# Performance work log

Hardware: AMD Instinct MI355X
Metric: run time of the kernel (lower is better)

Reference implementation:

```python
import jax, jax.numpy as jnp
import numpy as np

N = 100000   # nodes
E = 1600000  # edges per graph (avg degree 16)
H = 32       # hidden_dim
L = 5        # num_layers
NEG_SLOPE = 0.2
PRELU_W = 0.1


def setup_inputs() -> dict:
    key = jax.random.key(0)
    ks = jax.random.split(key, 32)
    nrm = lambda k, s: jax.random.normal(k, s, dtype=jnp.float32) * 0.1
    inp = {
        "x": jax.random.normal(ks[0], (N, 1), dtype=jnp.float32),
        "source_edge_index": jax.random.randint(ks[1], (2, E), 0, N, dtype=jnp.int64) if jax.config.jax_enable_x64 else jax.random.randint(ks[1], (2, E), 0, N, dtype=jnp.int32),
        "sink_edge_index": jax.random.randint(ks[2], (2, E), 0, N, dtype=jnp.int32),
        "W_in_src": nrm(ks[3], (1, H)), "b_in_src": nrm(ks[4], (H,)),
        "a1_in_src": nrm(ks[5], (H,)), "a2_in_src": nrm(ks[6], (H,)),
        "W_in_snk": nrm(ks[7], (1, H)), "b_in_snk": nrm(ks[8], (H,)),
        "a1_in_snk": nrm(ks[9], (H,)), "a2_in_snk": nrm(ks[10], (H,)),
        "W_src": nrm(ks[11], (L - 1, H, H)), "b_src": nrm(ks[12], (L - 1, H)),
        "a1_src": nrm(ks[13], (L - 1, H)), "a2_src": nrm(ks[14], (L - 1, H)),
        "W_snk": nrm(ks[15], (L - 1, H, H)), "b_snk": nrm(ks[16], (L - 1, H)),
        "a1_snk": nrm(ks[17], (L - 1, H)), "a2_snk": nrm(ks[18], (L - 1, H)),
        "W_o_src": nrm(ks[19], (2 * H, 2)), "b_o_src": nrm(ks[20], (2,)),
        "W_o_snk": nrm(ks[21], (2 * H, 2)), "b_o_snk": nrm(ks[22], (2,)),
        "W_d1": nrm(ks[23], (2 * H, 2)), "b_d1": nrm(ks[24], (2,)),
    }
    return inp


def _prelu(v):
    return jnp.where(v >= 0, v, PRELU_W * v)


def _gat(xf, ei, W, b, a1, a2):
    # single-head GATConv, concat=False: linear -> edge attention softmax over dst -> scatter-add
    h = xf @ W                                   # [N,H]
    s, d = ei[0], ei[1]
    e = jax.nn.leaky_relu((h @ a1)[s] + (h @ a2)[d], NEG_SLOPE)   # [E]
    m = jax.ops.segment_max(e, d, num_segments=N)
    m = jnp.where(jnp.isfinite(m), m, 0.0)
    p = jnp.exp(e - m[d])
    denom = jax.ops.segment_sum(p, d, num_segments=N)
    alpha = p / (denom[d] + 1e-16)
    out = jax.ops.segment_sum(alpha[:, None] * h[s], d, num_segments=N)
    return out + b


def _edge_neighbor(emb, ei, filt):
    # message: x_j * filt[src]; aggr='add'; update: aggr + emb/2
    s, d = ei[0], ei[1]
    agg = jax.ops.segment_sum(emb[s] * filt[s], d, num_segments=N)
    return agg + emb / 2


def reference(x, source_edge_index, sink_edge_index,
              W_in_src, b_in_src, a1_in_src, a2_in_src,
              W_in_snk, b_in_snk, a1_in_snk, a2_in_snk,
              W_src, b_src, a1_src, a2_src,
              W_snk, b_snk, a1_snk, a2_snk,
              W_o_src, b_o_src, W_o_snk, b_o_snk, W_d1, b_d1):
    # eval mode: dropout is identity
    se = _prelu(_gat(x, source_edge_index, W_in_src, b_in_src, a1_in_src, a2_in_src))
    sk = _prelu(_gat(x, sink_edge_index, W_in_snk, b_in_snk, a1_in_snk, a2_in_snk))
    for i in range(L - 1):
        c = se + sk   # combine='add'
        se = _prelu(_gat(c, source_edge_index, W_src[i], b_src[i], a1_src[i], a2_src[i]))
        sk = _prelu(_gat(c, sink_edge_index, W_snk[i], b_snk[i], a1_snk[i], a2_snk[i]))
    comb = jnp.concatenate([se, sk], axis=-1)     # [N, 2H] to match Linear(2H, 2)
    s0 = jax.nn.relu(comb @ W_o_src + b_o_src)
    k0 = jax.nn.relu(comb @ W_o_snk + b_o_snk)
    final_dim0 = (s0 + k0) / 2                    # [N, 2]
    e1s = jax.nn.relu(_edge_neighbor(comb, source_edge_index, x))
    e1k = jax.nn.relu(_edge_neighbor(comb, sink_edge_index, x))
    final_dim1 = jax.nn.relu((e1s + e1k) @ W_d1 + b_d1)   # [N, 2]
    return jnp.concatenate([final_dim0, final_dim1], axis=1)  # [N, 4]
```

## Files before the change

kernel.cpp:

```cpp
#include <hip/hip_runtime.h>

#define NEG_SLOPE 0.2f
#define PRELU_W 0.1f

__device__ __forceinline__ float d_lrelu(float v){ return fmaxf(v, NEG_SLOPE * v); }
__device__ __forceinline__ float d_prelu(float v){ return fmaxf(v, PRELU_W * v); }

__device__ __forceinline__ unsigned short f2bf(float f){
  unsigned int u = __builtin_bit_cast(unsigned int, f);
  unsigned int r = (u + 0x7fffu + ((u >> 16) & 1u)) >> 16;
  return (unsigned short)r;
}
__device__ __forceinline__ float bflo(unsigned int u){ return __builtin_bit_cast(float, u << 16); }
__device__ __forceinline__ float bfhi(unsigned int u){ return __builtin_bit_cast(float, u & 0xffff0000u); }


__global__ void k_zero(int* __restrict__ p, int n){
  int i = blockIdx.x * 256 + threadIdx.x;
  if (i < n) p[i] = 0;
}

__global__ void k_count_rank(const int* __restrict__ eiS, const int* __restrict__ eiK,
                             int* __restrict__ degS, int* __restrict__ degK,
                             int* __restrict__ rankS, int* __restrict__ rankK, int E){
  int e0 = blockIdx.x * 512 + threadIdx.x;
  int e1 = e0 + 256;
  bool v0 = e0 < E, v1 = e1 < E;
  int dS0 = 0, dK0 = 0, dS1 = 0, dK1 = 0;
  if (v0){ dS0 = eiS[E + e0]; dK0 = eiK[E + e0]; }
  if (v1){ dS1 = eiS[E + e1]; dK1 = eiK[E + e1]; }
  if (v0){
    rankS[e0] = atomicAdd(&degS[dS0], 1);
    rankK[e0] = atomicAdd(&degK[dK0], 1);
  }
  if (v1){
    rankS[e1] = atomicAdd(&degS[dS1], 1);
    rankK[e1] = atomicAdd(&degK[dK1], 1);
  }
}

__global__ void k_scan1(const int* __restrict__ degS, const int* __restrict__ degK,
                        int* __restrict__ bsumS, int* __restrict__ bsumK, int n){
  const int* deg = blockIdx.y ? degK : degS;
  int* bsum = blockIdx.y ? bsumK : bsumS;
  int b = blockIdx.x, t = threadIdx.x;
  int base = b * 1024 + t * 4;
  int s = 0;
  #pragma unroll
  for (int k2 = 0; k2 < 4; ++k2){ int i = base + k2; if (i < n) s += deg[i]; }
  #pragma unroll
  for (int d = 32; d >= 1; d >>= 1) s += __shfl_xor(s, d, 64);
  __shared__ int ws[4];
  int lane = t & 63, wid = t >> 6;
  if (lane == 0) ws[wid] = s;
  __syncthreads();
  if (t == 0) bsum[b] = ws[0] + ws[1] + ws[2] + ws[3];
}

__global__ void k_scan2(int* __restrict__ bsumS, int* __restrict__ bsumK, int nb,
                        int* __restrict__ rsS, int* __restrict__ rsK, int n){
  int* bsum = blockIdx.x ? bsumK : bsumS;
  int* rs = blockIdx.x ? rsK : rsS;
  int t = threadIdx.x;
  int v = (t < nb) ? bsum[t] : 0;
  int x = v;
  int lane = t & 63, wid = t >> 6;
  #pragma unroll
  for (int d = 1; d < 64; d <<= 1){ int y = __shfl_up(x, d, 64); if (lane >= d) x += y; }
  __shared__ int wq[2];
  if (lane == 63) wq[wid] = x;
  __syncthreads();
  if (wid == 1) x += wq[0];
  if (t < nb) bsum[t] = x - v;
  if (t == nb - 1) rs[n] = x;
}

__global__ void k_scan3(const int* __restrict__ degS, const int* __restrict__ degK,
                        const int* __restrict__ bsumS, const int* __restrict__ bsumK,
                        int* __restrict__ rsS, int* __restrict__ rsK, int n){
  const int* deg = blockIdx.y ? degK : degS;
  const int* bsum = blockIdx.y ? bsumK : bsumS;
  int* rs = blockIdx.y ? rsK : rsS;
  int b = blockIdx.x, t = threadIdx.x;
  int base = b * 1024 + t * 4;
  int v[4];
  #pragma unroll
  for (int k2 = 0; k2 < 4; ++k2){ int i = base + k2; v[k2] = (i < n) ? deg[i] : 0; }
  int tsum = v[0] + v[1] + v[2] + v[3];
  int x = tsum;
  int lane = t & 63, wid = t >> 6;
  #pragma unroll
  for (int d = 1; d < 64; d <<= 1){ int y = __shfl_up(x, d, 64); if (lane >= d) x += y; }
  __shared__ int ws[4];
  if (lane == 63) ws[wid] = x;
  __syncthreads();
  int woff = 0;
  for (int w = 0; w < wid; ++w) woff += ws[w];
  int run = bsum[b] + woff + (x - tsum);
  #pragma unroll
  for (int k2 = 0; k2 < 4; ++k2){ int i = base + k2; if (i < n) rs[i] = run; run += v[k2]; }
}

__global__ void k_place(const int* __restrict__ eiS, const int* __restrict__ eiK,
                        const int* __restrict__ rsS, const int* __restrict__ rsK,
                        const int* __restrict__ rankS, const int* __restrict__ rankK,
                        int* __restrict__ colS, int* __restrict__ colK, int E){
  int e0 = blockIdx.x * 512 + threadIdx.x;
  int e1 = e0 + 256;
  bool v0 = e0 < E, v1 = e1 < E;
  if (v0){
    int sS = eiS[e0], dS = eiS[E + e0];
    int sK = eiK[e0], dK = eiK[E + e0];
    int rS = rankS[e0], rK = rankK[e0];
    colS[rsS[dS] + rS] = sS;
    colK[rsK[dK] + rK] = sK;
  }
  if (v1){
    int sS = eiS[e1], dS = eiS[E + e1];
    int sK = eiK[e1], dK = eiK[E + e1];
    int rS = rankS[e1], rK = rankK[e1];
    colS[rsS[dS] + rS] = sS;
    colK[rsK[dK] + rK] = sK;
  }
}

__global__ void k_gat_l1(const int* __restrict__ rsA, const int* __restrict__ colA,
                         const int* __restrict__ rsB, const int* __restrict__ colB,
                         const float* __restrict__ x,
                         const float* __restrict__ WA, const float* __restrict__ bA,
                         const float* __restrict__ a1A, const float* __restrict__ a2A,
                         const float* __restrict__ WB, const float* __restrict__ bB,
                         const float* __restrict__ a1B, const float* __restrict__ a2B,
                         float* __restrict__ outA, float* __restrict__ outB, int n){
  bool g = (blockIdx.y != 0);
  const int* rs  = g ? rsB  : rsA;
  const int* col = g ? colB : colA;
  const float* W = g ? WB : WA;  const float* bias = g ? bB : bA;
  const float* a1 = g ? a1B : a1A; const float* a2 = g ? a2B : a2A;
  float* outp = g ? outB : outA;

  __shared__ float sp[2];
  int t = threadIdx.x;
  if (t < 32){
    float wk = W[t];
    float q1 = wk * a1[t], q2 = wk * a2[t];
    #pragma unroll
    for (int d = 16; d >= 1; d >>= 1){ q1 += __shfl_xor(q1, d, 32); q2 += __shfl_xor(q2, d, 32); }
    if (t == 0){ sp[0] = q1; sp[1] = q2; }
  }
  __syncthreads();
  float p1 = sp[0], p2 = sp[1];

  int gid = blockIdx.x * 256 + t;
  int node = gid >> 3, l8 = gid & 7;
  if (node >= n) return;
  float a2d = x[node] * p2;
  int beg = rs[node], end = rs[node + 1];
  float denom = 0.f, accx = 0.f;
  #pragma unroll 2
  for (int idx = beg + l8; idx < end; idx += 8){
    float xs = x[col[idx]];
    float w = __expf(d_lrelu(xs * p1 + a2d));
    denom += w;
    accx += w * xs;
  }
  #pragma unroll
  for (int d = 4; d >= 1; d >>= 1){
    denom += __shfl_xor(denom, d, 8);
    accx  += __shfl_xor(accx,  d, 8);
  }
  float r = accx / (denom + 1e-16f);
  float4 Wv = *(const float4*)(W + l8 * 4);
  float4 Bv = *(const float4*)(bias + l8 * 4);
  float4 o;
  o.x = d_prelu(r * Wv.x + Bv.x);
  o.y = d_prelu(r * Wv.y + Bv.y);
  o.z = d_prelu(r * Wv.z + Bv.z);
  o.w = d_prelu(r * Wv.w + Bv.w);
  *(float4*)(outp + (size_t)node * 32 + l8 * 4) = o;
}

__global__ void k_linear(const float* __restrict__ se, const float* __restrict__ sk,
                         const float* __restrict__ WS, const float* __restrict__ WK,
                         const float* __restrict__ a1S, const float* __restrict__ a2S,
                         const float* __restrict__ a1K, const float* __restrict__ a2K,
                         unsigned short* __restrict__ hS, unsigned short* __restrict__ hK,
                         float* __restrict__ oa1S, float* __restrict__ oa2S,
                         float* __restrict__ oa1K, float* __restrict__ oa2K, int n){
  __shared__ float sWS[1024], sWK[1024], sa[128];
  int t = threadIdx.x;
  for (int i = t; i < 1024; i += 256){ sWS[i] = WS[i]; sWK[i] = WK[i]; }
  if (t < 32){ sa[t] = a1S[t]; sa[32 + t] = a2S[t]; sa[64 + t] = a1K[t]; sa[96 + t] = a2K[t]; }
  __syncthreads();
  int gid = blockIdx.x * 256 + t;
  int node = gid >> 5, k = gid & 31;
  if (node >= n) return;
  float c = se[node * 32 + k] + sk[node * 32 + k];
  float hs = 0.f, hk = 0.f;
  #pragma unroll
  for (int m = 0; m < 32; ++m){
    float cm = __shfl(c, m, 32);
    hs += cm * sWS[m * 32 + k];
    hk += cm * sWK[m * 32 + k];
  }
  hS[node * 32 + k] = f2bf(hs);
  hK[node * 32 + k] = f2bf(hk);
  float r1 = hs * sa[k], r2 = hs * sa[32 + k], r3 = hk * sa[64 + k], r4 = hk * sa[96 + k];
  #pragma unroll
  for (int d = 16; d >= 1; d >>= 1){
    r1 += __shfl_xor(r1, d, 32); r2 += __shfl_xor(r2, d, 32);
    r3 += __shfl_xor(r3, d, 32); r4 += __shfl_xor(r4, d, 32);
  }
  if (k == 0){ oa1S[node] = r1; oa2S[node] = r2; oa1K[node] = r3; oa2K[node] = r4; }
}

__global__ void k_gat_agg(const int* __restrict__ rsA, const int* __restrict__ colA,
                          const unsigned short* __restrict__ hA,
                          const float* __restrict__ a1A, const float* __restrict__ a2A,
                          const float* __restrict__ bA, float* __restrict__ outA,
                          const int* __restrict__ rsB, const int* __restrict__ colB,
                          const unsigned short* __restrict__ hB,
                          const float* __restrict__ a1B, const float* __restrict__ a2B,
                          const float* __restrict__ bB, float* __restrict__ outB, int n){
  bool g2 = (blockIdx.y != 0);
  const int* rs  = g2 ? rsB  : rsA;
  const int* col = g2 ? colB : colA;
  const unsigned short* h = g2 ? hB : hA;
  const float* a1 = g2 ? a1B : a1A;
  const float* a2 = g2 ? a2B : a2A;
  const float* bias = g2 ? bB : bA;
  float* outp = g2 ? outB : outA;

  int t = threadIdx.x;
  int lane = t & 63;
  int half = lane >> 5, l32 = lane & 31;
  int node = blockIdx.x * 8 + (t >> 6) * 2 + half;
  if (node >= n) return;
  int g = l32 >> 2;
  int k = (l32 & 3) * 8;
  float a2d = a2[node];
  int beg = rs[node], end = rs[node + 1];
  float acc[8] = {0.f,0.f,0.f,0.f,0.f,0.f,0.f,0.f};
  float dpart = 0.f;
  #pragma unroll 2
  for (int idx = beg + g; idx < end; idx += 8){
    int s = col[idx];
    float w = __expf(d_lrelu(a1[s] + a2d));
    uint4 hv = *(const uint4*)(h + (((size_t)s) << 5) + k);
    dpart += w;
    acc[0] += w * bflo(hv.x); acc[1] += w * bfhi(hv.x);
    acc[2] += w * bflo(hv.y); acc[3] += w * bfhi(hv.y);
    acc[4] += w * bflo(hv.z); acc[5] += w * bfhi(hv.z);
    acc[6] += w * bflo(hv.w); acc[7] += w * bfhi(hv.w);
  }
  #pragma unroll
  for (int m = 4; m <= 16; m <<= 1){
    #pragma unroll
    for (int i = 0; i < 8; ++i) acc[i] += __shfl_xor(acc[i], m, 32);
    dpart += __shfl_xor(dpart, m, 32);
  }
  if (g == 0){
    float inv = 1.f / (dpart + 1e-16f);
    float4 b0 = *(const float4*)(bias + k);
    float4 b1 = *(const float4*)(bias + k + 4);
    float4 o0, o1;
    o0.x = d_prelu(acc[0] * inv + b0.x);
    o0.y = d_prelu(acc[1] * inv + b0.y);
    o0.z = d_prelu(acc[2] * inv + b0.z);
    o0.w = d_prelu(acc[3] * inv + b0.w);
    o1.x = d_prelu(acc[4] * inv + b1.x);
    o1.y = d_prelu(acc[5] * inv + b1.y);
    o1.z = d_prelu(acc[6] * inv + b1.z);
    o1.w = d_prelu(acc[7] * inv + b1.w);
    *(float4*)(outp + (size_t)node * 32 + k) = o0;
    *(float4*)(outp + (size_t)node * 32 + k + 4) = o1;
  }
}

__global__ void k_head0(const float* __restrict__ se, const float* __restrict__ sk,
                        const float* __restrict__ Wos, const float* __restrict__ bos,
                        const float* __restrict__ Wok, const float* __restrict__ bok,
                        unsigned short* __restrict__ comb, float* __restrict__ outp, int n){
  int gid = blockIdx.x * 256 + threadIdx.x;
  int node = gid >> 6, k = gid & 63;
  if (node >= n) return;
  float cv = (k < 32) ? se[node * 32 + k] : sk[node * 32 + (k - 32)];
  comb[(size_t)node * 64 + k] = f2bf(cv);
  float s0 = cv * Wos[k * 2], s1 = cv * Wos[k * 2 + 1];
  float q0 = cv * Wok[k * 2], q1 = cv * Wok[k * 2 + 1];
  #pragma unroll
  for (int d = 32; d >= 1; d >>= 1){
    s0 += __shfl_xor(s0, d, 64); s1 += __shfl_xor(s1, d, 64);
    q0 += __shfl_xor(q0, d, 64); q1 += __shfl_xor(q1, d, 64);
  }
  if (k == 0){
    float f0 = (fmaxf(s0 + bos[0], 0.f) + fmaxf(q0 + bok[0], 0.f)) * 0.5f;
    float f1 = (fmaxf(s1 + bos[1], 0.f) + fmaxf(q1 + bok[1], 0.f)) * 0.5f;
    outp[node * 4 + 0] = f0;
    outp[node * 4 + 1] = f1;
  }
}

__global__ void k_head1(const int* __restrict__ rsS, const int* __restrict__ colS,
                        const int* __restrict__ rsK, const int* __restrict__ colK,
                        const unsigned short* __restrict__ comb, const float* __restrict__ x,
                        const float* __restrict__ Wd1, const float* __restrict__ bd1,
                        float* __restrict__ outp, int n){
  int lane = threadIdx.x & 63;
  int node = blockIdx.x * 4 + (threadIdx.x >> 6);
  if (node >= n) return;
  int g8 = lane >> 3, k8 = (lane & 7) * 8;
  float aS[8] = {0.f,0.f,0.f,0.f,0.f,0.f,0.f,0.f};
  float aK[8] = {0.f,0.f,0.f,0.f,0.f,0.f,0.f,0.f};
  {
    int beg = rsS[node], end = rsS[node + 1];
    #pragma unroll 2
    for (int idx = beg + g8; idx < end; idx += 8){
      int s = colS[idx];
      float xs = x[s];
      uint4 cv = *(const uint4*)(comb + (((size_t)s) << 6) + k8);
      aS[0] += xs * bflo(cv.x); aS[1] += xs * bfhi(cv.x);
      aS[2] += xs * bflo(cv.y); aS[3] += xs * bfhi(cv.y);
      aS[4] += xs * bflo(cv.z); aS[5] += xs * bfhi(cv.z);
      aS[6] += xs * bflo(cv.w); aS[7] += xs * bfhi(cv.w);
    }
  }
  {
    int beg = rsK[node], end = rsK[node + 1];
    #pragma unroll 2
    for (int idx = beg + g8; idx < end; idx += 8){
      int s = colK[idx];
      float xs = x[s];
      uint4 cv = *(const uint4*)(comb + (((size_t)s) << 6) + k8);
      aK[0] += xs * bflo(cv.x); aK[1] += xs * bfhi(cv.x);
      aK[2] += xs * bflo(cv.y); aK[3] += xs * bfhi(cv.y);
      aK[4] += xs * bflo(cv.z); aK[5] += xs * bfhi(cv.z);
      aK[6] += xs * bflo(cv.w); aK[7] += xs * bfhi(cv.w);
    }
  }
  #pragma unroll
  for (int m = 8; m <= 32; m <<= 1){
    #pragma unroll
    for (int i = 0; i < 8; ++i){
      aS[i] += __shfl_xor(aS[i], m, 64);
      aK[i] += __shfl_xor(aK[i], m, 64);
    }
  }
  uint4 cs = *(const uint4*)(comb + (((size_t)node) << 6) + k8);
  float c[8] = { bflo(cs.x), bfhi(cs.x), bflo(cs.y), bfhi(cs.y),
                 bflo(cs.z), bfhi(cs.z), bflo(cs.w), bfhi(cs.w) };
  float r0 = 0.f, r1 = 0.f;
  #pragma unroll
  for (int i = 0; i < 8; ++i){
    float cd = c[i] * 0.5f;
    float tv = fmaxf(aS[i] + cd, 0.f) + fmaxf(aK[i] + cd, 0.f);
    float2 w = *(const float2*)(Wd1 + (k8 + i) * 2);
    r0 += tv * w.x;
    r1 += tv * w.y;
  }
  #pragma unroll
  for (int m = 1; m <= 4; m <<= 1){
    r0 += __shfl_xor(r0, m, 64);
    r1 += __shfl_xor(r1, m, 64);
  }
  if (lane == 0){
    outp[(size_t)node * 4 + 2] = fmaxf(r0 + bd1[0], 0.f);
    outp[(size_t)node * 4 + 3] = fmaxf(r1 + bd1[1], 0.f);
  }
}


extern "C" void kernel_launch(void* const* d_in, const int* in_sizes, int n_in,
                              void* d_out, int out_size, void* d_ws, size_t ws_size,
                              hipStream_t stream) {
  const float* x      = (const float*)d_in[0];
  const int*   eiS    = (const int*)d_in[1];
  const int*   eiK    = (const int*)d_in[2];
  const float* W_in_src = (const float*)d_in[3];
  const float* b_in_src = (const float*)d_in[4];
  const float* a1_in_src= (const float*)d_in[5];
  const float* a2_in_src= (const float*)d_in[6];
  const float* W_in_snk = (const float*)d_in[7];
  const float* b_in_snk = (const float*)d_in[8];
  const float* a1_in_snk= (const float*)d_in[9];
  const float* a2_in_snk= (const float*)d_in[10];
  const float* W_src  = (const float*)d_in[11];
  const float* b_src  = (const float*)d_in[12];
  const float* a1_src = (const float*)d_in[13];
  const float* a2_src = (const float*)d_in[14];
  const float* W_snk  = (const float*)d_in[15];
  const float* b_snk  = (const float*)d_in[16];
  const float* a1_snk = (const float*)d_in[17];
  const float* a2_snk = (const float*)d_in[18];
  const float* W_o_src= (const float*)d_in[19];
  const float* b_o_src= (const float*)d_in[20];
  const float* W_o_snk= (const float*)d_in[21];
  const float* b_o_snk= (const float*)d_in[22];
  const float* W_d1   = (const float*)d_in[23];
  const float* b_d1   = (const float*)d_in[24];
  float* outp = (float*)d_out;

  const int N = in_sizes[0];
  const int E = in_sizes[1] / 2;
  const int L = 5;

  float* f = (float*)d_ws;
  float* seA = f;  f += (size_t)N * 32;
  float* skA = f;  f += (size_t)N * 32;
  float* a1Sv = f; f += N;
  float* a2Sv = f; f += N;
  float* a1Kv = f; f += N;
  float* a2Kv = f; f += N;
  int* ip = (int*)f;
  int* rsS    = ip; ip += N + 4;
  int* rsK    = ip; ip += N + 4;
  int* colS   = ip; ip += E;
  int* colK   = ip; ip += E;
  int* degS   = ip; ip += N;
  int* degK   = ip; ip += N;
  int* bsumS  = ip; ip += 256;
  int* bsumK  = ip; ip += 256;
  unsigned short* us = (unsigned short*)ip;
  unsigned short* hS   = us; us += (size_t)N * 32;
  unsigned short* hK   = us; us += (size_t)N * 32;
  unsigned short* comb = us; us += (size_t)N * 64;
  int* rankS = (int*)hS;
  int* rankK = (int*)hK;

  const int TB = 256;
  int gE2   = (E + 511) / 512;
  int gN32  = (N * 32 + TB - 1) / TB;
  int gN64  = (N * 64 + TB - 1) / TB;
  int gN8   = (N * 8 + TB - 1) / TB;
  int gNode4 = (N + 3) / 4;
  int gNode8 = (N + 7) / 8;
  int nb    = (N + 1023) / 1024;

  hipLaunchKernelGGL(k_zero,  dim3((2 * N + TB - 1) / TB), dim3(TB), 0, stream, degS, 2 * N);
  hipLaunchKernelGGL(k_count_rank, dim3(gE2), dim3(TB), 0, stream,
                     eiS, eiK, degS, degK, rankS, rankK, E);
  hipLaunchKernelGGL(k_scan1, dim3(nb, 2), dim3(TB), 0, stream, degS, degK, bsumS, bsumK, N);
  hipLaunchKernelGGL(k_scan2, dim3(2), dim3(128), 0, stream, bsumS, bsumK, nb, rsS, rsK, N);
  hipLaunchKernelGGL(k_scan3, dim3(nb, 2), dim3(TB), 0, stream,
                     degS, degK, bsumS, bsumK, rsS, rsK, N);
  hipLaunchKernelGGL(k_place, dim3(gE2), dim3(TB), 0, stream,
                     eiS, eiK, rsS, rsK, rankS, rankK, colS, colK, E);

  hipLaunchKernelGGL(k_gat_l1, dim3(gN8, 2), dim3(TB), 0, stream,
                     rsS, colS, rsK, colK, x,
                     W_in_src, b_in_src, a1_in_src, a2_in_src,
                     W_in_snk, b_in_snk, a1_in_snk, a2_in_snk,
                     seA, skA, N);

  for (int i = 0; i < L - 1; ++i){
    hipLaunchKernelGGL(k_linear, dim3(gN32), dim3(TB), 0, stream,
                       seA, skA, W_src + (size_t)i * 1024, W_snk + (size_t)i * 1024,
                       a1_src + i * 32, a2_src + i * 32, a1_snk + i * 32, a2_snk + i * 32,
                       hS, hK, a1Sv, a2Sv, a1Kv, a2Kv, N);
    hipLaunchKernelGGL(k_gat_agg, dim3(gNode8, 2), dim3(TB), 0, stream,
                       rsS, colS, hS, a1Sv, a2Sv, b_src + i * 32, seA,
                       rsK, colK, hK, a1Kv, a2Kv, b_snk + i * 32, skA, N);
  }

  hipLaunchKernelGGL(k_head0, dim3(gN64), dim3(TB), 0, stream,
                     seA, skA, W_o_src, b_o_src, W_o_snk, b_o_snk, comb, outp, N);
  hipLaunchKernelGGL(k_head1, dim3(gNode4), dim3(TB), 0, stream,
                     rsS, colS, rsK, colK, comb, x, W_d1, b_d1, outp, N);
}
```

Before: 851.8 us.

## Partition CSR build atomics by destination range per XCD and drop rank arrays

Reworks the CSR construction. Each block now handles one of eight destination-node ranges, so the atomics for a given range come from a predictable subset of blocks, which the block-index mapping presumably ties to one XCD for cache locality. The rank arrays are gone: the placement kernel uses atomic cursors that the scan initialises to the row starts. Each block now reads edges eight times over, and the order of neighbours within a row becomes nondeterministic.

```diff
diff --git a/kernel.cpp b/kernel.cpp
--- a/kernel.cpp
+++ b/kernel.cpp
@@ -20,22 +20,23 @@
   if (i < n) p[i] = 0;
 }
 
-__global__ void k_count_rank(const int* __restrict__ eiS, const int* __restrict__ eiK,
-                             int* __restrict__ degS, int* __restrict__ degK,
-                             int* __restrict__ rankS, int* __restrict__ rankK, int E){
-  int e0 = blockIdx.x * 512 + threadIdx.x;
-  int e1 = e0 + 256;
-  bool v0 = e0 < E, v1 = e1 < E;
-  int dS0 = 0, dK0 = 0, dS1 = 0, dK1 = 0;
-  if (v0){ dS0 = eiS[E + e0]; dK0 = eiK[E + e0]; }
-  if (v1){ dS1 = eiS[E + e1]; dK1 = eiK[E + e1]; }
-  if (v0){
-    rankS[e0] = atomicAdd(&degS[dS0], 1);
-    rankK[e0] = atomicAdd(&degK[dK0], 1);
-  }
-  if (v1){
-    rankS[e1] = atomicAdd(&degS[dS1], 1);
-    rankK[e1] = atomicAdd(&degK[dK1], 1);
+__global__ void k_count_x(const int* __restrict__ eiS, const int* __restrict__ eiK,
+                          int* __restrict__ degS, int* __restrict__ degK,
+                          int E, int rngN, int n){
+  int r = blockIdx.x & 7;
+  int c = blockIdx.x >> 3;
+  int lo = r * rngN;
+  int hi = min(lo + rngN, n);
+  int base = c * 2048 + threadIdx.x;
+  #pragma unroll
+  for (int i = 0; i < 8; ++i){
+    int e = base + i * 256;
+    if (e < E){
+      int dS = eiS[E + e];
+      if (dS >= lo && dS < hi) atomicAdd(&degS[dS], 1);
+      int dK = eiK[E + e];
+      if (dK >= lo && dK < hi) atomicAdd(&degK[dK], 1);
+    }
   }
 }
 
@@ -75,10 +76,10 @@
   if (t == nb - 1) rs[n] = x;
 }
 
-__global__ void k_scan3(const int* __restrict__ degS, const int* __restrict__ degK,
+__global__ void k_scan3(int* __restrict__ degS, int* __restrict__ degK,
                         const int* __restrict__ bsumS, const int* __restrict__ bsumK,
                         int* __restrict__ rsS, int* __restrict__ rsK, int n){
-  const int* deg = blockIdx.y ? degK : degS;
+  int* deg = blockIdx.y ? degK : degS;
   const int* bsum = blockIdx.y ? bsumK : bsumS;
   int* rs = blockIdx.y ? rsK : rsS;
   int b = blockIdx.x, t = threadIdx.x;
@@ -98,29 +99,37 @@
   for (int w = 0; w < wid; ++w) woff += ws[w];
   int run = bsum[b] + woff + (x - tsum);
   #pragma unroll
-  for (int k2 = 0; k2 < 4; ++k2){ int i = base + k2; if (i < n) rs[i] = run; run += v[k2]; }
-}
-
-__global__ void k_place(const int* __restrict__ eiS, const int* __restrict__ eiK,
-                        const int* __restrict__ rsS, const int* __restrict__ rsK,
-                        const int* __restrict__ rankS, const int* __restrict__ rankK,
-                        int* __restrict__ colS, int* __restrict__ colK, int E){
-  int e0 = blockIdx.x * 512 + threadIdx.x;
-  int e1 = e0 + 256;
-  bool v0 = e0 < E, v1 = e1 < E;
-  if (v0){
-    int sS = eiS[e0], dS = eiS[E + e0];
-    int sK = eiK[e0], dK = eiK[E + e0];
-    int rS = rankS[e0], rK = rankK[e0];
-    colS[rsS[dS] + rS] = sS;
-    colK[rsK[dK] + rK] = sK;
-  }
-  if (v1){
-    int sS = eiS[e1], dS = eiS[E + e1];
-    int sK = eiK[e1], dK = eiK[E + e1];
-    int rS = rankS[e1], rK = rankK[e1];
-    colS[rsS[dS] + rS] = sS;
-    colK[rsK[dK] + rK] = sK;
+  for (int k2 = 0; k2 < 4; ++k2){
+    int i = base + k2;
+    if (i < n){ rs[i] = run; deg[i] = run; }
+    run += v[k2];
+  }
+}
+
+__global__ void k_place_x(const int* __restrict__ eiS, const int* __restrict__ eiK,
+                          int* __restrict__ curS, int* __restrict__ curK,
+                          int* __restrict__ colS, int* __restrict__ colK,
+                          int E, int rngN, int n){
+  int r = blockIdx.x & 7;
+  int c = blockIdx.x >> 3;
+  int lo = r * rngN;
+  int hi = min(lo + rngN, n);
+  int base = c * 2048 + threadIdx.x;
+  #pragma unroll
+  for (int i = 0; i < 8; ++i){
+    int e = base + i * 256;
+    if (e < E){
+      int dS = eiS[E + e];
+      if (dS >= lo && dS < hi){
+        int p = atomicAdd(&curS[dS], 1);
+        colS[p] = eiS[e];
+      }
+      int dK = eiK[E + e];
+      if (dK >= lo && dK < hi){
+        int p = atomicAdd(&curK[dK], 1);
+        colK[p] = eiK[e];
+      }
+    }
   }
 }
 
@@ -424,11 +433,10 @@
   unsigned short* hS   = us; us += (size_t)N * 32;
   unsigned short* hK   = us; us += (size_t)N * 32;
   unsigned short* comb = us; us += (size_t)N * 64;
-  int* rankS = (int*)hS;
-  int* rankK = (int*)hK;
 
   const int TB = 256;
-  int gE2   = (E + 511) / 512;
+  int rngN  = (N + 7) / 8;
+  int gCX   = ((E + 2047) / 2048) * 8;
   int gN32  = (N * 32 + TB - 1) / TB;
   int gN64  = (N * 64 + TB - 1) / TB;
   int gN8   = (N * 8 + TB - 1) / TB;
@@ -437,14 +445,14 @@
   int nb    = (N + 1023) / 1024;
 
   hipLaunchKernelGGL(k_zero,  dim3((2 * N + TB - 1) / TB), dim3(TB), 0, stream, degS, 2 * N);
-  hipLaunchKernelGGL(k_count_rank, dim3(gE2), dim3(TB), 0, stream,
-                     eiS, eiK, degS, degK, rankS, rankK, E);
+  hipLaunchKernelGGL(k_count_x, dim3(gCX), dim3(TB), 0, stream,
+                     eiS, eiK, degS, degK, E, rngN, N);
   hipLaunchKernelGGL(k_scan1, dim3(nb, 2), dim3(TB), 0, stream, degS, degK, bsumS, bsumK, N);
   hipLaunchKernelGGL(k_scan2, dim3(2), dim3(128), 0, stream, bsumS, bsumK, nb, rsS, rsK, N);
   hipLaunchKernelGGL(k_scan3, dim3(nb, 2), dim3(TB), 0, stream,
                      degS, degK, bsumS, bsumK, rsS, rsK, N);
-  hipLaunchKernelGGL(k_place, dim3(gE2), dim3(TB), 0, stream,
-                     eiS, eiK, rsS, rsK, rankS, rankK, colS, colK, E);
+  hipLaunchKernelGGL(k_place_x, dim3(gCX), dim3(TB), 0, stream,
+                     eiS, eiK, degS, degK, colS, colK, E, rngN, N);
 
   hipLaunchKernelGGL(k_gat_l1, dim3(gN8, 2), dim3(TB), 0, stream,
                      rsS, colS, rsK, colK, x,
```

Result: slower. 942.5 us (+10.7%).

## Partition degree-count atomics by destination range across block groups

Applied to the files above, without the earlier changes.

The in-degree counting and rank kernel now launches eight blocks per 2048-edge chunk. Each of the eight handles only destinations in one of eight node ranges, so each block's atomics land in a narrower slice of the degree array. This is meant to keep the atomic targets local to a cache or XCD and cut cross-die atomic contention. In exchange, every edge index is read eight times and most threads do nothing for a given edge.

```diff
diff --git a/kernel.cpp b/kernel.cpp
--- a/kernel.cpp
+++ b/kernel.cpp
@@ -20,22 +20,24 @@
   if (i < n) p[i] = 0;
 }
 
-__global__ void k_count_rank(const int* __restrict__ eiS, const int* __restrict__ eiK,
-                             int* __restrict__ degS, int* __restrict__ degK,
-                             int* __restrict__ rankS, int* __restrict__ rankK, int E){
-  int e0 = blockIdx.x * 512 + threadIdx.x;
-  int e1 = e0 + 256;
-  bool v0 = e0 < E, v1 = e1 < E;
-  int dS0 = 0, dK0 = 0, dS1 = 0, dK1 = 0;
-  if (v0){ dS0 = eiS[E + e0]; dK0 = eiK[E + e0]; }
-  if (v1){ dS1 = eiS[E + e1]; dK1 = eiK[E + e1]; }
-  if (v0){
-    rankS[e0] = atomicAdd(&degS[dS0], 1);
-    rankK[e0] = atomicAdd(&degK[dK0], 1);
-  }
-  if (v1){
-    rankS[e1] = atomicAdd(&degS[dS1], 1);
-    rankK[e1] = atomicAdd(&degK[dK1], 1);
+__global__ void k_count_rank_x(const int* __restrict__ eiS, const int* __restrict__ eiK,
+                               int* __restrict__ degS, int* __restrict__ degK,
+                               int* __restrict__ rankS, int* __restrict__ rankK,
+                               int E, int rngN, int n){
+  int r = blockIdx.x & 7;
+  int c = blockIdx.x >> 3;
+  int lo = r * rngN;
+  int hi = min(lo + rngN, n);
+  int base = c * 2048 + threadIdx.x;
+  #pragma unroll
+  for (int i = 0; i < 8; ++i){
+    int e = base + i * 256;
+    if (e < E){
+      int dS = eiS[E + e];
+      if (dS >= lo && dS < hi) rankS[e] = atomicAdd(&degS[dS], 1);
+      int dK = eiK[E + e];
+      if (dK >= lo && dK < hi) rankK[e] = atomicAdd(&degK[dK], 1);
+    }
   }
 }
 
@@ -428,6 +430,8 @@
   int* rankK = (int*)hK;
 
   const int TB = 256;
+  int rngN  = (N + 7) / 8;
+  int gCX   = ((E + 2047) / 2048) * 8;
   int gE2   = (E + 511) / 512;
   int gN32  = (N * 32 + TB - 1) / TB;
   int gN64  = (N * 64 + TB - 1) / TB;
@@ -437,8 +441,8 @@
   int nb    = (N + 1023) / 1024;
 
   hipLaunchKernelGGL(k_zero,  dim3((2 * N + TB - 1) / TB), dim3(TB), 0, stream, degS, 2 * N);
-  hipLaunchKernelGGL(k_count_rank, dim3(gE2), dim3(TB), 0, stream,
-                     eiS, eiK, degS, degK, rankS, rankK, E);
+  hipLaunchKernelGGL(k_count_rank_x, dim3(gCX), dim3(TB), 0, stream,
+                     eiS, eiK, degS, degK, rankS, rankK, E, rngN, N);
   hipLaunchKernelGGL(k_scan1, dim3(nb, 2), dim3(TB), 0, stream, degS, degK, bsumS, bsumK, N);
   hipLaunchKernelGGL(k_scan2, dim3(2), dim3(128), 0, stream, bsumS, bsumK, nb, rsS, rsK, N);
   hipLaunchKernelGGL(k_scan3, dim3(nb, 2), dim3(TB), 0, stream,
```

Result: no change. 857.8 us (+0.7%).

## Stage block edge indices and attention weights in LDS before gather

Applied to the files above, without the earlier changes.

The GAT aggregation and head1 neighbor kernels now load each block's contiguous CSR edge segment cooperatively. One thread per edge reads the column index and computes the attention weight (or x value) once, and stores them in shared memory. Each half-wave then reads those from LDS while gathering feature rows. Before, every one of the four lanes per edge recomputed the exp and reloaded col and a1. This removes that redundant global and transcendental work and coalesces the index reads, at the cost of extra __syncthreads and LDS traffic.

```diff
diff --git a/kernel.cpp b/kernel.cpp
--- a/kernel.cpp
+++ b/kernel.cpp
@@ -214,66 +214,103 @@
   if (k == 0){ oa1S[node] = r1; oa2S[node] = r2; oa1K[node] = r3; oa2K[node] = r4; }
 }
 
-__global__ void k_gat_agg(const int* __restrict__ rsA, const int* __restrict__ colA,
-                          const unsigned short* __restrict__ hA,
-                          const float* __restrict__ a1A, const float* __restrict__ a2A,
-                          const float* __restrict__ bA, float* __restrict__ outA,
-                          const int* __restrict__ rsB, const int* __restrict__ colB,
-                          const unsigned short* __restrict__ hB,
-                          const float* __restrict__ a1B, const float* __restrict__ a2B,
-                          const float* __restrict__ bB, float* __restrict__ outB, int n){
-  bool g2 = (blockIdx.y != 0);
-  const int* rs  = g2 ? rsB  : rsA;
-  const int* col = g2 ? colB : colA;
-  const unsigned short* h = g2 ? hB : hA;
-  const float* a1 = g2 ? a1B : a1A;
-  const float* a2 = g2 ? a2B : a2A;
-  const float* bias = g2 ? bB : bA;
-  float* outp = g2 ? outB : outA;
+__global__ void k_gat_agg2(const int* __restrict__ rsA, const int* __restrict__ colA,
+                           const unsigned short* __restrict__ hA,
+                           const float* __restrict__ a1A, const float* __restrict__ a2A,
+                           const float* __restrict__ bA, float* __restrict__ outA,
+                           const int* __restrict__ rsB, const int* __restrict__ colB,
+                           const unsigned short* __restrict__ hB,
+                           const float* __restrict__ a1B, const float* __restrict__ a2B,
+                           const float* __restrict__ bB, float* __restrict__ outB, int n){
+  bool gB = (blockIdx.y != 0);
+  const int* rs  = gB ? rsB  : rsA;
+  const int* col = gB ? colB : colA;
+  const unsigned short* h = gB ? hB : hA;
+  const float* a1 = gB ? a1B : a1A;
+  const float* a2 = gB ? a2B : a2A;
+  const float* bias = gB ? bB : bA;
+  float* outp = gB ? outB : outA;
+
+  __shared__ int rsL[9];
+  __shared__ int sC[256];
+  __shared__ float wC[256];
 
   int t = threadIdx.x;
+  int n0 = blockIdx.x * 8;
+  if (t < 9){
+    int idx = n0 + t;
+    rsL[t] = rs[idx < n ? idx : n];
+  }
+  __syncthreads();
+  int seg0 = rsL[0], segEnd = rsL[8];
+
   int lane = t & 63;
   int half = lane >> 5, l32 = lane & 31;
-  int node = blockIdx.x * 8 + (t >> 6) * 2 + half;
-  if (node >= n) return;
+  int nl = (t >> 6) * 2 + half;
+  int node = n0 + nl;
   int g = l32 >> 2;
   int k = (l32 & 3) * 8;
-  float a2d = a2[node];
-  int beg = rs[node], end = rs[node + 1];
+  int myBeg = rsL[nl], myEnd = rsL[nl + 1];
+  int deg = myEnd - myBeg;
+  float a2d = (node < n) ? a2[node] : 0.f;
+
   float acc[8] = {0.f,0.f,0.f,0.f,0.f,0.f,0.f,0.f};
   float dpart = 0.f;
-  #pragma unroll 2
-  for (int idx = beg + g; idx < end; idx += 8){
-    int s = col[idx];
-    float w = __expf(d_lrelu(a1[s] + a2d));
-    uint4 hv = *(const uint4*)(h + (((size_t)s) << 5) + k);
-    dpart += w;
-    acc[0] += w * bflo(hv.x); acc[1] += w * bfhi(hv.x);
-    acc[2] += w * bflo(hv.y); acc[3] += w * bfhi(hv.y);
-    acc[4] += w * bflo(hv.z); acc[5] += w * bfhi(hv.z);
-    acc[6] += w * bflo(hv.w); acc[7] += w * bfhi(hv.w);
-  }
+
+  for (int base = seg0; base < segEnd; base += 256){
+    int j = base + t;
+    int sv = 0; float wv = 0.f;
+    bool val = j < segEnd;
+    if (val){
+      sv = col[j];
+      int dl = 0;
+      #pragma unroll
+      for (int i = 1; i < 8; ++i) dl += (j >= rsL[i]);
+      wv = __expf(d_lrelu(a1[sv] + a2[n0 + dl]));
+    }
+    __syncthreads();
+    if (val){ sC[t] = sv; wC[t] = wv; }
+    __syncthreads();
+    int lo = (myBeg > base) ? myBeg : base;
+    int hi = (myEnd < base + 256) ? myEnd : (base + 256);
+    int o0 = lo - myBeg;
+    int r8 = o0 & 7;
+    int ord = o0 + ((g - r8) & 7);
+    #pragma unroll 2
+    for (; myBeg + ord < hi; ord += 8){
+      int li = myBeg + ord - base;
+      int s = sC[li];
+      float w = wC[li];
+      uint4 hv = *(const uint4*)(h + (((size_t)s) << 5) + k);
+      dpart += w;
+      acc[0] += w * bflo(hv.x); acc[1] += w * bfhi(hv.x);
+      acc[2] += w * bflo(hv.y); acc[3] += w * bfhi(hv.y);
+      acc[4] += w * bflo(hv.z); acc[5] += w * bfhi(hv.z);
+      acc[6] += w * bflo(hv.w); acc[7] += w * bfhi(hv.w);
+    }
+  }
+
   #pragma unroll
   for (int m = 4; m <= 16; m <<= 1){
     #pragma unroll
     for (int i = 0; i < 8; ++i) acc[i] += __shfl_xor(acc[i], m, 32);
     dpart += __shfl_xor(dpart, m, 32);
   }
-  if (g == 0){
+  if (g == 0 && node < n){
     float inv = 1.f / (dpart + 1e-16f);
     float4 b0 = *(const float4*)(bias + k);
     float4 b1 = *(const float4*)(bias + k + 4);
-    float4 o0, o1;
-    o0.x = d_prelu(acc[0] * inv + b0.x);
-    o0.y = d_prelu(acc[1] * inv + b0.y);
-    o0.z = d_prelu(acc[2] * inv + b0.z);
-    o0.w = d_prelu(acc[3] * inv + b0.w);
-    o1.x = d_prelu(acc[4] * inv + b1.x);
-    o1.y = d_prelu(acc[5] * inv + b1.y);
-    o1.z = d_prelu(acc[6] * inv + b1.z);
-    o1.w = d_prelu(acc[7] * inv + b1.w);
-    *(float4*)(outp + (size_t)node * 32 + k) = o0;
-    *(float4*)(outp + (size_t)node * 32 + k + 4) = o1;
+    float4 o0v, o1v;
+    o0v.x = d_prelu(acc[0] * inv + b0.x);
+    o0v.y = d_prelu(acc[1] * inv + b0.y);
+    o0v.z = d_prelu(acc[2] * inv + b0.z);
+    o0v.w = d_prelu(acc[3] * inv + b0.w);
+    o1v.x = d_prelu(acc[4] * inv + b1.x);
+    o1v.y = d_prelu(acc[5] * inv + b1.y);
+    o1v.z = d_prelu(acc[6] * inv + b1.z);
+    o1v.w = d_prelu(acc[7] * inv + b1.w);
+    *(float4*)(outp + (size_t)node * 32 + k) = o0v;
+    *(float4*)(outp + (size_t)node * 32 + k + 4) = o1v;
   }
 }
 
@@ -301,43 +338,64 @@
   }
 }
 
-__global__ void k_head1(const int* __restrict__ rsS, const int* __restrict__ colS,
-                        const int* __restrict__ rsK, const int* __restrict__ colK,
-                        const unsigned short* __restrict__ comb, const float* __restrict__ x,
-                        const float* __restrict__ Wd1, const float* __restrict__ bd1,
-                        float* __restrict__ outp, int n){
-  int lane = threadIdx.x & 63;
-  int node = blockIdx.x * 4 + (threadIdx.x >> 6);
-  if (node >= n) return;
+__global__ void k_head1b(const int* __restrict__ rsS, const int* __restrict__ colS,
+                         const int* __restrict__ rsK, const int* __restrict__ colK,
+                         const unsigned short* __restrict__ comb, const float* __restrict__ x,
+                         const float* __restrict__ Wd1, const float* __restrict__ bd1,
+                         float* __restrict__ outp, int n){
+  __shared__ int rsL[5];
+  __shared__ int sC[256];
+  __shared__ float xC[256];
+
+  int t = threadIdx.x;
+  int n0 = blockIdx.x * 4;
+  int lane = t & 63;
+  int nl = t >> 6;
+  int node = n0 + nl;
   int g8 = lane >> 3, k8 = (lane & 7) * 8;
+
   float aS[8] = {0.f,0.f,0.f,0.f,0.f,0.f,0.f,0.f};
   float aK[8] = {0.f,0.f,0.f,0.f,0.f,0.f,0.f,0.f};
-  {
-    int beg = rsS[node], end = rsS[node + 1];
-    #pragma unroll 2
-    for (int idx = beg + g8; idx < end; idx += 8){
-      int s = colS[idx];
-      float xs = x[s];
-      uint4 cv = *(const uint4*)(comb + (((size_t)s) << 6) + k8);
-      aS[0] += xs * bflo(cv.x); aS[1] += xs * bfhi(cv.x);
-      aS[2] += xs * bflo(cv.y); aS[3] += xs * bfhi(cv.y);
-      aS[4] += xs * bflo(cv.z); aS[5] += xs * bfhi(cv.z);
-      aS[6] += xs * bflo(cv.w); aS[7] += xs * bfhi(cv.w);
-    }
-  }
-  {
-    int beg = rsK[node], end = rsK[node + 1];
-    #pragma unroll 2
-    for (int idx = beg + g8; idx < end; idx += 8){
-      int s = colK[idx];
-      float xs = x[s];
-      uint4 cv = *(const uint4*)(comb + (((size_t)s) << 6) + k8);
-      aK[0] += xs * bflo(cv.x); aK[1] += xs * bfhi(cv.x);
-      aK[2] += xs * bflo(cv.y); aK[3] += xs * bfhi(cv.y);
-      aK[4] += xs * bflo(cv.z); aK[5] += xs * bfhi(cv.z);
-      aK[6] += xs * bflo(cv.w); aK[7] += xs * bfhi(cv.w);
-    }
-  }
+
+  for (int gr = 0; gr < 2; ++gr){
+    const int* rs  = gr ? rsK : rsS;
+    const int* col = gr ? colK : colS;
+    float* acc = gr ? aK : aS;
+    __syncthreads();
+    if (t < 5){
+      int idx = n0 + t;
+      rsL[t] = rs[idx < n ? idx : n];
+    }
+    __syncthreads();
+    int seg0 = rsL[0], segEnd = rsL[4];
+    int myBeg = rsL[nl], myEnd = rsL[nl + 1];
+    for (int base = seg0; base < segEnd; base += 256){
+      int j = base + t;
+      int sv = 0; float xv = 0.f;
+      bool val = j < segEnd;
+      if (val){ sv = col[j]; xv = x[sv]; }
+      __syncthreads();
+      if (val){ sC[t] = sv; xC[t] = xv; }
+      __syncthreads();
+      int lo = (myBeg > base) ? myBeg : base;
+      int hi = (myEnd < base + 256) ? myEnd : (base + 256);
+      int o0 = lo - myBeg;
+      int r8 = o0 & 7;
+      int ord = o0 + ((g8 - r8) & 7);
+      #pragma unroll 2
+      for (; myBeg + ord < hi; ord += 8){
+        int li = myBeg + ord - base;
+        int s = sC[li];
+        float xs = xC[li];
+        uint4 cv = *(const uint4*)(comb + (((size_t)s) << 6) + k8);
+        acc[0] += xs * bflo(cv.x); acc[1] += xs * bfhi(cv.x);
+        acc[2] += xs * bflo(cv.y); acc[3] += xs * bfhi(cv.y);
+        acc[4] += xs * bflo(cv.z); acc[5] += xs * bfhi(cv.z);
+        acc[6] += xs * bflo(cv.w); acc[7] += xs * bfhi(cv.w);
+      }
+    }
+  }
+
   #pragma unroll
   for (int m = 8; m <= 32; m <<= 1){
     #pragma unroll
@@ -346,26 +404,28 @@
       aK[i] += __shfl_xor(aK[i], m, 64);
     }
   }
-  uint4 cs = *(const uint4*)(comb + (((size_t)node) << 6) + k8);
-  float c[8] = { bflo(cs.x), bfhi(cs.x), bflo(cs.y), bfhi(cs.y),
-                 bflo(cs.z), bfhi(cs.z), bflo(cs.w), bfhi(cs.w) };
-  float r0 = 0.f, r1 = 0.f;
-  #pragma unroll
-  for (int i = 0; i < 8; ++i){
-    float cd = c[i] * 0.5f;
-    float tv = fmaxf(aS[i] + cd, 0.f) + fmaxf(aK[i] + cd, 0.f);
-    float2 w = *(const float2*)(Wd1 + (k8 + i) * 2);
-    r0 += tv * w.x;
-    r1 += tv * w.y;
-  }
-  #pragma unroll
-  for (int m = 1; m <= 4; m <<= 1){
-    r0 += __shfl_xor(r0, m, 64);
-    r1 += __shfl_xor(r1, m, 64);
-  }
-  if (lane == 0){
-    outp[(size_t)node * 4 + 2] = fmaxf(r0 + bd1[0], 0.f);
-    outp[(size_t)node * 4 + 3] = fmaxf(r1 + bd1[1], 0.f);
+  if (node < n){
+    uint4 cs = *(const uint4*)(comb + (((size_t)node) << 6) + k8);
+    float c[8] = { bflo(cs.x), bfhi(cs.x), bflo(cs.y), bfhi(cs.y),
+                   bflo(cs.z), bfhi(cs.z), bflo(cs.w), bfhi(cs.w) };
+    float r0 = 0.f, r1 = 0.f;
+    #pragma unroll
+    for (int i = 0; i < 8; ++i){
+      float cd = c[i] * 0.5f;
+      float tv = fmaxf(aS[i] + cd, 0.f) + fmaxf(aK[i] + cd, 0.f);
+      float2 w = *(const float2*)(Wd1 + (k8 + i) * 2);
+      r0 += tv * w.x;
+      r1 += tv * w.y;
+    }
+    #pragma unroll
+    for (int m = 1; m <= 4; m <<= 1){
+      r0 += __shfl_xor(r0, m, 64);
+      r1 += __shfl_xor(r1, m, 64);
+    }
+    if (lane == 0){
+      outp[(size_t)node * 4 + 2] = fmaxf(r0 + bd1[0], 0.f);
+      outp[(size_t)node * 4 + 3] = fmaxf(r1 + bd1[1], 0.f);
+    }
   }
 }
 
@@ -432,8 +492,8 @@
   int gN32  = (N * 32 + TB - 1) / TB;
   int gN64  = (N * 64 + TB - 1) / TB;
   int gN8   = (N * 8 + TB - 1) / TB;
+  int gNode8 = (N + 7) / 8;
   int gNode4 = (N + 3) / 4;
-  int gNode8 = (N + 7) / 8;
   int nb    = (N + 1023) / 1024;
 
   hipLaunchKernelGGL(k_zero,  dim3((2 * N + TB - 1) / TB), dim3(TB), 0, stream, degS, 2 * N);
@@ -457,13 +517,13 @@
                        seA, skA, W_src + (size_t)i * 1024, W_snk + (size_t)i * 1024,
                        a1_src + i * 32, a2_src + i * 32, a1_snk + i * 32, a2_snk + i * 32,
                        hS, hK, a1Sv, a2Sv, a1Kv, a2Kv, N);
-    hipLaunchKernelGGL(k_gat_agg, dim3(gNode8, 2), dim3(TB), 0, stream,
+    hipLaunchKernelGGL(k_gat_agg2, dim3(gNode8, 2), dim3(TB), 0, stream,
                        rsS, colS, hS, a1Sv, a2Sv, b_src + i * 32, seA,
                        rsK, colK, hK, a1Kv, a2Kv, b_snk + i * 32, skA, N);
   }
 
   hipLaunchKernelGGL(k_head0, dim3(gN64), dim3(TB), 0, stream,
                      seA, skA, W_o_src, b_o_src, W_o_snk, b_o_snk, comb, outp, N);
-  hipLaunchKernelGGL(k_head1, dim3(gNode4), dim3(TB), 0, stream,
+  hipLaunchKernelGGL(k_head1b, dim3(gNode4), dim3(TB), 0, stream,
                      rsS, colS, rsK, colK, comb, x, W_d1, b_d1, outp, N);
 }
```

New measurement: 858.8 us. Within noise of the previous version (+0.8%).
